# Performance work log

Hardware: AMD Instinct MI355X
Metric: run time of the kernel (lower is better)

## Reference

```python
import jax, jax.numpy as jnp
import numpy as np

H, W = 32, 32
DIM = 768
NUM_BLOCKS = 4
BLOCK = DIM // NUM_BLOCKS
SCALE = 0.02


def setup_inputs() -> dict:
    key = jax.random.key(0)
    k0, k1, k2, k3, k4 = jax.random.split(key, 5)
    B, N, C = 64, H * W, DIM
    x = jax.random.normal(k0, (B, N, C), dtype=jnp.float32)
    w1 = SCALE * jax.random.normal(k1, (2, NUM_BLOCKS, BLOCK, BLOCK), dtype=jnp.float32)
    b1 = SCALE * jax.random.normal(k2, (2, NUM_BLOCKS, BLOCK), dtype=jnp.float32)
    w2 = SCALE * jax.random.normal(k3, (2, NUM_BLOCKS, BLOCK, BLOCK), dtype=jnp.float32)
    b2 = SCALE * jax.random.normal(k4, (2, NUM_BLOCKS, BLOCK), dtype=jnp.float32)
    return {"x": x, "w1": w1, "b1": b1, "w2": w2, "b2": b2}


def _mul(inp, weights):
    # inp: [B, H, Wf, blocks, d], weights: [blocks, d, k]
    return jnp.einsum('...bd,bdk->...bk', inp, weights)


def reference(x, w1, b1, w2, b2):
    B, N, C = x.shape
    xg = x.reshape(B, H, W, C)
    xf = jnp.fft.rfft2(xg, axes=(1, 2), norm='ortho')  # [B, H, W//2+1, C] complex64
    xf = xf.reshape(B, xf.shape[1], xf.shape[2], NUM_BLOCKS, BLOCK)
    xr, xi = xf.real, xf.imag
    # layer 1: complex block-diagonal linear + ReLU
    r1 = jax.nn.relu(_mul(xr, w1[0]) - _mul(xi, w1[1]) + b1[0])
    i1 = jax.nn.relu(_mul(xr, w1[1]) + _mul(xi, w1[0]) + b1[1])
    # layer 2 (faithful to original: imag uses the already-updated real part)
    r2 = _mul(r1, w2[0]) - _mul(i1, w2[1]) + b2[0]
    i2 = _mul(r2, w2[1]) + _mul(i1, w2[0]) + b2[1]
    xc = (r2 + 1j * i2).reshape(B, r2.shape[1], r2.shape[2], C)
    out = jnp.fft.irfft2(xc, s=(H, W), axes=(1, 2), norm='ortho')
    return out.reshape(B, N, C) + jnp.zeros_like(x)  # bias is zeros (self.bias is None)
```

## Files before the change

### kernel.cpp

```cpp
#include <hip/hip_runtime.h>
#include <cstddef>
#include <cstdint>


typedef __attribute__((ext_vector_type(8))) short bf16x8;
typedef __attribute__((ext_vector_type(4))) float f32x4;

namespace {

constexpr int BATCH = 64;
constexpr int WF    = 17;
constexpr int CC    = 768;
constexpr int BLK   = 192;

constexpr size_t W_ELEMS  = 16u * 36864u;
constexpr size_t TW_ELEMS = 8u * 1024u;
constexpr size_t PW_ELEMS = W_ELEMS + TW_ELEMS;

constexpr int PLANE_U = 48 * 512;

constexpr float C32[32] = {
   1.0000000000f,  0.9807852804f,  0.9238795325f,  0.8314696123f,
   0.7071067812f,  0.5555702330f,  0.3826834324f,  0.1950903220f,
   0.0000000000f, -0.1950903220f, -0.3826834324f, -0.5555702330f,
  -0.7071067812f, -0.8314696123f, -0.9238795325f, -0.9807852804f,
  -1.0000000000f, -0.9807852804f, -0.9238795325f, -0.8314696123f,
  -0.7071067812f, -0.5555702330f, -0.3826834324f, -0.1950903220f,
   0.0000000000f,  0.1950903220f,  0.3826834324f,  0.5555702330f,
   0.7071067812f,  0.8314696123f,  0.9238795325f,  0.9807852804f
};
constexpr float S32[32] = {
   0.0000000000f,  0.1950903220f,  0.3826834324f,  0.5555702330f,
   0.7071067812f,  0.8314696123f,  0.9238795325f,  0.9807852804f,
   1.0000000000f,  0.9807852804f,  0.9238795325f,  0.8314696123f,
   0.7071067812f,  0.5555702330f,  0.3826834324f,  0.1950903220f,
   0.0000000000f, -0.1950903220f, -0.3826834324f, -0.5555702330f,
  -0.7071067812f, -0.8314696123f, -0.9238795325f, -0.9807852804f,
  -1.0000000000f, -0.9807852804f, -0.9238795325f, -0.8314696123f,
  -0.7071067812f, -0.5555702330f, -0.3826834324f, -0.1950903220f
};

}

__device__ __forceinline__ ushort f2bf(float f) {
    union { float f; unsigned u; } v; v.f = f;
    const unsigned r = (v.u + 0x7FFFu + ((v.u >> 16) & 1u)) >> 16;
    return (ushort)r;
}
__device__ __forceinline__ uint pk(float lo, float hi) {
    return (uint)f2bf(lo) | ((uint)f2bf(hi) << 16);
}
__device__ __forceinline__ bf16x8 neg8(bf16x8 a) {
    union { bf16x8 v; uint4 u; } t; t.v = a;
    t.u.x ^= 0x80008000u; t.u.y ^= 0x80008000u;
    t.u.z ^= 0x80008000u; t.u.w ^= 0x80008000u;
    return t.v;
}

__global__ __launch_bounds__(256) void k_pack(const float* __restrict__ w1,
                                              const float* __restrict__ w2,
                                              ushort* __restrict__ pw) {
    const unsigned idx = blockIdx.x * 256u + threadIdx.x;
    if (idx < W_ELEMS) {
        const unsigned mi = idx / 36864u;
        const unsigned r  = idx % 36864u;
        const unsigned kk = r / 6144u;
        const unsigned r2 = r % 6144u;
        const unsigned nf = r2 / 512u;
        const unsigned r3 = r2 % 512u;
        const unsigned lane = r3 / 8u;
        const unsigned i  = r3 % 8u;
        const unsigned d   = kk * 32u + (lane >> 4) * 8u + i;
        const unsigned col = nf * 16u + (lane & 15u);
        const unsigned mat = mi >> 2, blk = mi & 3u;
        const float* src;
        if      (mat == 0u) src = w1 + (size_t)(0 * 4 + blk) * BLK * BLK;
        else if (mat == 1u) src = w1 + (size_t)(1 * 4 + blk) * BLK * BLK;
        else if (mat == 2u) src = w2 + (size_t)(0 * 4 + blk) * BLK * BLK;
        else                src = w2 + (size_t)(1 * 4 + blk) * BLK * BLK;
        pw[idx] = f2bf(src[(size_t)d * BLK + col]);
    } else if (idx < PW_ELEMS) {
        const unsigned t = idx - (unsigned)W_ELEMS;
        const unsigned mat = t >> 10;
        const unsigned rr  = t & 1023u;
        const unsigned mf  = rr >> 9;
        const unsigned q   = rr & 511u;
        const unsigned lane = q >> 3, i = q & 7u;
        const unsigned row = mf * 16u + (lane & 15u);
        const unsigned col = (lane >> 4) * 8u + i;
        const unsigned ang = (row * col) & 31u;
        float v;
        if      (mat == 0u) v = C32[ang] * 0.03125f;
        else if (mat == 1u) v = S32[ang] * 0.03125f;
        else if (mat == 2u) v = -S32[ang] * 0.03125f;
        else if (mat == 3u) v = C32[ang];
        else if (mat == 4u) v = S32[ang];
        else if (mat == 5u) v = -S32[ang];
        else if (mat == 6u) {
            if      (col == 0u)  v = 0.03125f;
            else if (col < 16u)  v = 2.f * C32[ang] * 0.03125f;
            else if (col == 16u) v = C32[(16u * row) & 31u] * 0.03125f;
            else                 v = 0.f;
        } else {
            v = (col >= 1u && col <= 15u) ? (-2.f * S32[ang] * 0.03125f) : 0.f;
        }
        pw[idx] = f2bf(v);
    }
}

__global__ __launch_bounds__(256) void k_rfft_w(const float* __restrict__ x,
                                                ushort* __restrict__ spec,
                                                const ushort* __restrict__ pw) {
    __shared__ uint xb[16 * 384];

    const int bid = blockIdx.x;
    const int cq = bid & 3;
    const int hp = (bid >> 2) & 15;
    const int b  = bid >> 6;
    const int tid = threadIdx.x;
    const int wv = tid >> 6, l = tid & 63, lc = l & 15, lg = l >> 4;

#pragma unroll
    for (int it = 0; it < 6; ++it) {
        const int flat = it * 256 + tid;
        const int h  = flat / 768;
        const int rm = flat % 768;
        const int wp = rm / 48;
        const int c4 = rm % 48;
        const float* p = x + ((size_t)(b * 1024 + (hp * 2 + h) * 32 + wp * 2) * CC)
                           + cq * 192 + c4 * 4;
        const float4 a  = *(const float4*)p;
        const float4 bb = *(const float4*)(p + CC);
        uint4 u;
        u.x = pk(a.x, bb.x); u.y = pk(a.y, bb.y);
        u.z = pk(a.z, bb.z); u.w = pk(a.w, bb.w);
        const int col = (h * 192 + c4 * 4) ^ (((wp >> 2) & 3) << 3);
        *(uint4*)&xb[wp * 384 + col] = u;
    }
    __syncthreads();

    const ushort* TW = pw + W_ELEMS;
    bf16x8 ac[2], as[2];
#pragma unroll
    for (int m = 0; m < 2; ++m) {
        ac[m] = *(const bf16x8*)(TW + ((size_t)(3 * 2 + m) * 64 + l) * 8);
        as[m] = *(const bf16x8*)(TW + ((size_t)(5 * 2 + m) * 64 + l) * 8);
    }

    f32x4 aR[2][6] = {}, aI[2][6] = {};
#pragma unroll
    for (int j = 0; j < 6; ++j) {
        const int nf = (j < 3) ? (wv * 3 + j) : (12 + wv * 3 + (j - 3));
        union { bf16x8 v; uint d[4]; } u;
#pragma unroll
        for (int t = 0; t < 4; ++t) {
            const int wp = lg * 4 + t;
            u.d[t] = xb[wp * 384 + ((nf * 16 + lc) ^ (lg << 3))];
        }
#pragma unroll
        for (int m = 0; m < 2; ++m) {
            aR[m][j] = __builtin_amdgcn_mfma_f32_16x16x32_bf16(ac[m], u.v, aR[m][j], 0, 0, 0);
            aI[m][j] = __builtin_amdgcn_mfma_f32_16x16x32_bf16(as[m], u.v, aI[m][j], 0, 0, 0);
        }
    }

    uint* spec32 = (uint*)spec;
    const int swz = (hp & 7) << 1;
#pragma unroll
    for (int m = 0; m < 2; ++m)
#pragma unroll
        for (int j = 0; j < 3; ++j)
#pragma unroll
            for (int r = 0; r < 4; ++r) {
                if (m == 1 && (lg != 0 || r != 0)) continue;
                const int kw = m * 16 + lg * 4 + r;
                const int csub = cq * 12 + wv * 3 + j;
                const size_t pos = ((size_t)(b * WF + kw) * 2) * 12288
                                 + csub * 256 + hp * 16 + (lc ^ swz);
                spec32[pos]         = pk(aR[m][j][r], aR[m][j + 3][r]);
                spec32[pos + 12288] = pk(aI[m][j][r], aI[m][j + 3][r]);
            }
}

__global__ __launch_bounds__(256, 4) void k_fft_mix(
        ushort* __restrict__ spec,
        const ushort* __restrict__ pw,
        const float* __restrict__ b1, const float* __restrict__ b2) {

    __shared__ ushort lds[3][6336];

    const int bid = blockIdx.x;
    const int blk = bid / (BATCH * WF);
    const int rem = bid % (BATCH * WF);
    const int b   = rem / WF;
    const int kw  = rem % WF;
    const int tid = threadIdx.x;
    const int wv = tid >> 6, l = tid & 63, lc = l & 15, lg = l >> 4;

    const size_t gR = ((size_t)(b * WF + kw) * 2) * PLANE_U + blk * 6144;
    const size_t gI = gR + PLANE_U;

#pragma unroll
    for (int j = 0; j < 3; ++j) {
        const int q = tid + 256 * j;
        const int dst = (q >> 6) * 528 + (q & 63) * 8;
        *(uint4*)&lds[0][dst] = *(const uint4*)(spec + gR + q * 8);
        *(uint4*)&lds[1][dst] = *(const uint4*)(spec + gI + q * 8);
    }
    __syncthreads();

    const ushort* TW = pw + W_ELEMS;
    const int col0 = wv * 48;

    {
        bf16x8 xr[3], xi[3];
#pragma unroll
        for (int n = 0; n < 3; ++n) {
            const int csub = wv * 3 + n;
            union { bf16x8 v; uint d[4]; } ur, ui;
#pragma unroll
            for (int t = 0; t < 4; ++t) {
                const int hp = lg * 4 + t;
                const int pos = csub * 528 + hp * 32 + ((lc ^ ((hp & 7) << 1)) << 1);
                ur.d[t] = *(const uint*)&lds[0][pos];
                ui.d[t] = *(const uint*)&lds[1][pos];
            }
            xr[n] = ur.v; xi[n] = ui.v;
        }
        bf16x8 cf[2], sf[2], sfn[2];
#pragma unroll
        for (int m = 0; m < 2; ++m) {
            cf[m]  = *(const bf16x8*)(TW + ((size_t)(0 * 2 + m) * 64 + l) * 8);
            sf[m]  = *(const bf16x8*)(TW + ((size_t)(1 * 2 + m) * 64 + l) * 8);
            sfn[m] = *(const bf16x8*)(TW + ((size_t)(2 * 2 + m) * 64 + l) * 8);
        }
        f32x4 yr[2][3] = {}, yi[2][3] = {};
#pragma unroll
        for (int m = 0; m < 2; ++m)
#pragma unroll
            for (int n = 0; n < 3; ++n) {
                yr[m][n] = __builtin_amdgcn_mfma_f32_16x16x32_bf16(cf[m],  xr[n], yr[m][n], 0, 0, 0);
                yr[m][n] = __builtin_amdgcn_mfma_f32_16x16x32_bf16(sf[m],  xi[n], yr[m][n], 0, 0, 0);
                yi[m][n] = __builtin_amdgcn_mfma_f32_16x16x32_bf16(cf[m],  xi[n], yi[m][n], 0, 0, 0);
                yi[m][n] = __builtin_amdgcn_mfma_f32_16x16x32_bf16(sfn[m], xr[n], yi[m][n], 0, 0, 0);
            }
#pragma unroll
        for (int m = 0; m < 2; ++m)
#pragma unroll
            for (int n = 0; n < 3; ++n)
#pragma unroll
                for (int rp = 0; rp < 2; ++rp) {
                    const uint ur = pk(yr[m][n][2 * rp], yr[m][n][2 * rp + 1]);
                    const uint ui = pk(yi[m][n][2 * rp], yi[m][n][2 * rp + 1]);
                    const int p0 = (wv * 3 + n) * 528 + (m * 16 + lg * 4 + 2 * rp) * 16 + lc;
                    lds[0][p0] = (ushort)ur; lds[0][p0 + 16] = (ushort)(ur >> 16);
                    lds[1][p0] = (ushort)ui; lds[1][p0 + 16] = (ushort)(ui >> 16);
                }
    }
    __syncthreads();

    const ushort* pW1r = pw + (size_t)(0 * 4 + blk) * 36864;
    const ushort* pW1i = pw + (size_t)(1 * 4 + blk) * 36864;
    const ushort* pW2r = pw + (size_t)(2 * 4 + blk) * 36864;
    const ushort* pW2i = pw + (size_t)(3 * 4 + blk) * 36864;

    {
        f32x4 aR[2][3], aI[2][3];
#pragma unroll
        for (int n = 0; n < 3; ++n) {
            const float br = b1[(size_t)(0 * 4 + blk) * BLK + col0 + n * 16 + lc];
            const float bi = b1[(size_t)(1 * 4 + blk) * BLK + col0 + n * 16 + lc];
#pragma unroll
            for (int m = 0; m < 2; ++m) {
                aR[m][n] = (f32x4){br, br, br, br};
                aI[m][n] = (f32x4){bi, bi, bi, bi};
            }
        }
#pragma unroll
        for (int kk = 0; kk < 6; ++kk) {
            const int csubA = 2 * kk + (lg >> 1);
            const int apos  = csubA * 528 + lc * 16 + (lg & 1) * 8;
            bf16x8 ar[2], ai[2], ain[2];
#pragma unroll
            for (int m = 0; m < 2; ++m) {
                ar[m]  = *(const bf16x8*)&lds[0][apos + m * 256];
                ai[m]  = *(const bf16x8*)&lds[1][apos + m * 256];
                ain[m] = neg8(ai[m]);
            }
            bf16x8 wr[3], wi[3];
#pragma unroll
            for (int n = 0; n < 3; ++n) {
                const size_t off = ((size_t)(kk * 12 + wv * 3 + n) * 64 + l) * 8;
                wr[n] = *(const bf16x8*)(pW1r + off);
                wi[n] = *(const bf16x8*)(pW1i + off);
            }
#pragma unroll
            for (int m = 0; m < 2; ++m)
#pragma unroll
                for (int n = 0; n < 3; ++n) {
                    aR[m][n] = __builtin_amdgcn_mfma_f32_16x16x32_bf16(ar[m],  wr[n], aR[m][n], 0, 0, 0);
                    aR[m][n] = __builtin_amdgcn_mfma_f32_16x16x32_bf16(ain[m], wi[n], aR[m][n], 0, 0, 0);
                    aI[m][n] = __builtin_amdgcn_mfma_f32_16x16x32_bf16(ar[m],  wi[n], aI[m][n], 0, 0, 0);
                    aI[m][n] = __builtin_amdgcn_mfma_f32_16x16x32_bf16(ai[m],  wr[n], aI[m][n], 0, 0, 0);
                }
        }
        __syncthreads();
#pragma unroll
        for (int m = 0; m < 2; ++m)
#pragma unroll
            for (int n = 0; n < 3; ++n)
#pragma unroll
                for (int rp = 0; rp < 2; ++rp) {
                    const uint ur = pk(fmaxf(aR[m][n][2 * rp], 0.f), fmaxf(aR[m][n][2 * rp + 1], 0.f));
                    const uint ui = pk(fmaxf(aI[m][n][2 * rp], 0.f), fmaxf(aI[m][n][2 * rp + 1], 0.f));
                    const int p0 = (wv * 3 + n) * 528 + (m * 16 + lg * 4 + 2 * rp) * 16 + lc;
                    lds[0][p0] = (ushort)ur; lds[0][p0 + 16] = (ushort)(ur >> 16);
                    lds[1][p0] = (ushort)ui; lds[1][p0 + 16] = (ushort)(ui >> 16);
                }
    }
    __syncthreads();

    {
        f32x4 cR[2][3];
#pragma unroll
        for (int n = 0; n < 3; ++n) {
            const float br = b2[(size_t)(0 * 4 + blk) * BLK + col0 + n * 16 + lc];
#pragma unroll
            for (int m = 0; m < 2; ++m) cR[m][n] = (f32x4){br, br, br, br};
        }
#pragma unroll
        for (int kk = 0; kk < 6; ++kk) {
            const int csubA = 2 * kk + (lg >> 1);
            const int apos  = csubA * 528 + lc * 16 + (lg & 1) * 8;
            bf16x8 ar[2], ain[2];
#pragma unroll
            for (int m = 0; m < 2; ++m) {
                ar[m]  = *(const bf16x8*)&lds[0][apos + m * 256];
                ain[m] = neg8(*(const bf16x8*)&lds[1][apos + m * 256]);
            }
            bf16x8 wr[3], wi[3];
#pragma unroll
            for (int n = 0; n < 3; ++n) {
                const size_t off = ((size_t)(kk * 12 + wv * 3 + n) * 64 + l) * 8;
                wr[n] = *(const bf16x8*)(pW2r + off);
                wi[n] = *(const bf16x8*)(pW2i + off);
            }
#pragma unroll
            for (int m = 0; m < 2; ++m)
#pragma unroll
                for (int n = 0; n < 3; ++n) {
                    cR[m][n] = __builtin_amdgcn_mfma_f32_16x16x32_bf16(ar[m],  wr[n], cR[m][n], 0, 0, 0);
                    cR[m][n] = __builtin_amdgcn_mfma_f32_16x16x32_bf16(ain[m], wi[n], cR[m][n], 0, 0, 0);
                }
        }
        __syncthreads();
#pragma unroll
        for (int m = 0; m < 2; ++m)
#pragma unroll
            for (int n = 0; n < 3; ++n) {
                const int csub = wv * 3 + n;
#pragma unroll
                for (int rp = 0; rp < 2; ++rp) {
                    const uint p = pk(cR[m][n][2 * rp], cR[m][n][2 * rp + 1]);
                    const int kh0 = m * 16 + lg * 4 + 2 * rp;
                    lds[0][csub * 528 + kh0 * 16 + lc]       = (ushort)p;
                    lds[0][csub * 528 + (kh0 + 1) * 16 + lc] = (ushort)(p >> 16);
                    const int hp = kh0 >> 1;
                    const int post = csub * 528 + hp * 32 + ((lc ^ ((hp & 7) << 1)) << 1);
                    *(uint*)&lds[2][post] = p;
                }
            }
    }
    __syncthreads();

    {
        f32x4 cI[2][3];
#pragma unroll
        for (int n = 0; n < 3; ++n) {
            const float bi = b2[(size_t)(1 * 4 + blk) * BLK + col0 + n * 16 + lc];
#pragma unroll
            for (int m = 0; m < 2; ++m) cI[m][n] = (f32x4){bi, bi, bi, bi};
        }
#pragma unroll
        for (int kk = 0; kk < 6; ++kk) {
            const int csubA = 2 * kk + (lg >> 1);
            const int apos  = csubA * 528 + lc * 16 + (lg & 1) * 8;
            bf16x8 a2[2], i1[2];
#pragma unroll
            for (int m = 0; m < 2; ++m) {
                a2[m] = *(const bf16x8*)&lds[0][apos + m * 256];
                i1[m] = *(const bf16x8*)&lds[1][apos + m * 256];
            }
            bf16x8 wi[3], wr[3];
#pragma unroll
            for (int n = 0; n < 3; ++n) {
                const size_t off = ((size_t)(kk * 12 + wv * 3 + n) * 64 + l) * 8;
                wi[n] = *(const bf16x8*)(pW2i + off);
                wr[n] = *(const bf16x8*)(pW2r + off);
            }
#pragma unroll
            for (int m = 0; m < 2; ++m)
#pragma unroll
                for (int n = 0; n < 3; ++n) {
                    cI[m][n] = __builtin_amdgcn_mfma_f32_16x16x32_bf16(a2[m], wi[n], cI[m][n], 0, 0, 0);
                    cI[m][n] = __builtin_amdgcn_mfma_f32_16x16x32_bf16(i1[m], wr[n], cI[m][n], 0, 0, 0);
                }
        }
        __syncthreads();
#pragma unroll
        for (int m = 0; m < 2; ++m)
#pragma unroll
            for (int n = 0; n < 3; ++n) {
                const int csub = wv * 3 + n;
#pragma unroll
                for (int rp = 0; rp < 2; ++rp) {
                    const int hp = (m * 16 + lg * 4 + 2 * rp) >> 1;
                    const int post = csub * 528 + hp * 32 + ((lc ^ ((hp & 7) << 1)) << 1);
                    *(uint*)&lds[1][post] = pk(cI[m][n][2 * rp], cI[m][n][2 * rp + 1]);
                }
            }
    }

    {
        bf16x8 ci[2], si[2], sn[2];
#pragma unroll
        for (int m = 0; m < 2; ++m) {
            ci[m] = *(const bf16x8*)(TW + ((size_t)(3 * 2 + m) * 64 + l) * 8);
            si[m] = *(const bf16x8*)(TW + ((size_t)(4 * 2 + m) * 64 + l) * 8);
            sn[m] = *(const bf16x8*)(TW + ((size_t)(5 * 2 + m) * 64 + l) * 8);
        }
        bf16x8 r2b[3], i2b[3];
#pragma unroll
        for (int n = 0; n < 3; ++n) {
            const int csub = wv * 3 + n;
            union { bf16x8 v; uint d[4]; } ur, ui;
#pragma unroll
            for (int t = 0; t < 4; ++t) {
                const int hp = lg * 4 + t;
                const int pos = csub * 528 + hp * 32 + ((lc ^ ((hp & 7) << 1)) << 1);
                ur.d[t] = *(const uint*)&lds[2][pos];
                ui.d[t] = *(const uint*)&lds[1][pos];
            }
            r2b[n] = ur.v; i2b[n] = ui.v;
        }
        f32x4 zr[2][3] = {}, zi[2][3] = {};
#pragma unroll
        for (int m = 0; m < 2; ++m)
#pragma unroll
            for (int n = 0; n < 3; ++n) {
                zr[m][n] = __builtin_amdgcn_mfma_f32_16x16x32_bf16(ci[m], r2b[n], zr[m][n], 0, 0, 0);
                zr[m][n] = __builtin_amdgcn_mfma_f32_16x16x32_bf16(sn[m], i2b[n], zr[m][n], 0, 0, 0);
                zi[m][n] = __builtin_amdgcn_mfma_f32_16x16x32_bf16(ci[m], i2b[n], zi[m][n], 0, 0, 0);
                zi[m][n] = __builtin_amdgcn_mfma_f32_16x16x32_bf16(si[m], r2b[n], zi[m][n], 0, 0, 0);
            }
#pragma unroll
        for (int m = 0; m < 2; ++m)
#pragma unroll
            for (int n = 0; n < 3; ++n) {
                const size_t cbase = gR + (size_t)(wv * 3 + n) * 512;
#pragma unroll
                for (int rp = 0; rp < 2; ++rp) {
                    const int hp = (m * 16 + lg * 4 + 2 * rp) >> 1;
                    const size_t pos = cbase + hp * 32 + ((lc ^ ((hp & 7) << 1)) << 1);
                    *(uint*)(spec + pos)           = pk(zr[m][n][2 * rp], zr[m][n][2 * rp + 1]);
                    *(uint*)(spec + pos + PLANE_U) = pk(zi[m][n][2 * rp], zi[m][n][2 * rp + 1]);
                }
            }
    }
}

__global__ __launch_bounds__(256) void k_irfft_w(const ushort* __restrict__ spec,
                                                 float* __restrict__ out,
                                                 const ushort* __restrict__ pw) {
    __shared__ uint rawR[17 * 198];
    __shared__ uint rawI[17 * 198];

    const int bid = blockIdx.x;
    const int cq = bid & 3;
    const int hp = (bid >> 2) & 15;
    const int b  = bid >> 6;
    const int tid = threadIdx.x;
    const int wv = tid >> 6, l = tid & 63, lc = l & 15, lg = l >> 4;

    const uint* spec32 = (const uint*)spec;

#pragma unroll
    for (int it = 0; it < 13; ++it) {
        const int slot = it * 256 + tid;
        if (slot < 3264) {
            const int part = slot & 7;
            const int c2   = slot >> 3;
            const int plane = c2 / 204;
            const int q  = c2 % 204;
            const int kw = q / 12, csub = q % 12;
            const size_t gpos = ((size_t)(b * WF + kw) * 2 + plane) * 12288
                              + (cq * 12 + csub) * 256 + hp * 16 + part * 2;
            const uint2 v = *(const uint2*)(spec32 + gpos);
            uint* dst = plane ? rawI : rawR;
            *(uint2*)&dst[kw * 198 + csub * 16 + part * 2] = v;
        }
    }
    __syncthreads();

    const ushort* TW = pw + W_ELEMS;
    bf16x8 twA[2], twB[2];
#pragma unroll
    for (int m = 0; m < 2; ++m) {
        twA[m] = *(const bf16x8*)(TW + ((size_t)(6 * 2 + m) * 64 + l) * 8);
        twB[m] = *(const bf16x8*)(TW + ((size_t)(7 * 2 + m) * 64 + l) * 8);
    }

    int rowoff[8];
#pragma unroll
    for (int i = 0; i < 8; ++i) {
        int kwv = lg * 8 + i;
        if (kwv > 16) kwv = 16;
        rowoff[i] = kwv * 396;
    }

    const ushort* rr = (const ushort*)rawR;
    const ushort* ri = (const ushort*)rawI;
    const int swz = (hp & 7) << 1;

    f32x4 acc[2][6] = {};
#pragma unroll
    for (int j = 0; j < 6; ++j) {
        const int coll = (wv * 6 + j) * 16 + lc;
        const int h  = coll & 1;
        const int cL = coll >> 1;
        const int bu = ((cL >> 4) * 16 + ((cL & 15) ^ swz)) * 2 + h;
        union { bf16x8 v; ushort s[8]; } fr, fi;
#pragma unroll
        for (int i = 0; i < 8; ++i) {
            fr.s[i] = rr[rowoff[i] + bu];
            fi.s[i] = ri[rowoff[i] + bu];
        }
#pragma unroll
        for (int m = 0; m < 2; ++m) {
            acc[m][j] = __builtin_amdgcn_mfma_f32_16x16x32_bf16(twA[m], fr.v, acc[m][j], 0, 0, 0);
            acc[m][j] = __builtin_amdgcn_mfma_f32_16x16x32_bf16(twB[m], fi.v, acc[m][j], 0, 0, 0);
        }
    }

#pragma unroll
    for (int m = 0; m < 2; ++m)
#pragma unroll
        for (int j = 0; j < 6; ++j) {
            const int coll = (wv * 6 + j) * 16 + lc;
            const int h  = coll & 1;
            const int c  = cq * 192 + (coll >> 1);
#pragma unroll
            for (int r = 0; r < 4; ++r) {
                const int w = m * 16 + lg * 4 + r;
                out[((size_t)(b * 1024 + (hp * 2 + h) * 32 + w)) * CC + c] = acc[m][j][r];
            }
        }
}

extern "C" void kernel_launch(void* const* d_in, const int* in_sizes, int n_in,
                              void* d_out, int out_size, void* d_ws, size_t ws_size,
                              hipStream_t stream) {
    const float* x  = (const float*)d_in[0];
    const float* w1 = (const float*)d_in[1];
    const float* b1 = (const float*)d_in[2];
    const float* w2 = (const float*)d_in[3];
    const float* b2 = (const float*)d_in[4];
    float* out = (float*)d_out;

    ushort* pw   = (ushort*)d_ws;
    ushort* spec = pw + PW_ELEMS;

    k_pack<<<dim3((unsigned)(PW_ELEMS / 256)), dim3(256), 0, stream>>>(w1, w2, pw);
    k_rfft_w<<<dim3(BATCH * 16 * 4), dim3(256), 0, stream>>>(x, spec, pw);
    k_fft_mix<<<dim3(4 * BATCH * WF), dim3(256), 0, stream>>>(spec, pw, b1, b2);
    k_irfft_w<<<dim3(BATCH * 16 * 4), dim3(256), 0, stream>>>(spec, out, pw);
}
```

Measured before the change: 285.5 us.

## Add fourth LDS buffer to drop barriers; derive negated twiddles in registers

Grows the fused spectral-mix kernel's shared memory from three to four bf16 planes so layer-1 outputs go to separate buffers. This lets two __syncthreads after the layer-2 GEMM loops be removed, since writes no longer overwrite data other waves may still be reading. It also drops the occupancy hint from launch_bounds and computes negated sine twiddles with neg8 instead of loading them. The larger LDS footprint and missing occupancy hint may cut the number of resident blocks per CU.

```diff
diff --git a/kernel.cpp b/kernel.cpp
--- a/kernel.cpp
+++ b/kernel.cpp
@@ -182,12 +182,12 @@
             }
 }
 
-__global__ __launch_bounds__(256, 4) void k_fft_mix(
+__global__ __launch_bounds__(256) void k_fft_mix(
         ushort* __restrict__ spec,
         const ushort* __restrict__ pw,
         const float* __restrict__ b1, const float* __restrict__ b2) {
 
-    __shared__ ushort lds[3][6336];
+    __shared__ ushort lds[4][6336];
 
     const int bid = blockIdx.x;
     const int blk = bid / (BATCH * WF);
@@ -232,7 +232,7 @@
         for (int m = 0; m < 2; ++m) {
             cf[m]  = *(const bf16x8*)(TW + ((size_t)(0 * 2 + m) * 64 + l) * 8);
             sf[m]  = *(const bf16x8*)(TW + ((size_t)(1 * 2 + m) * 64 + l) * 8);
-            sfn[m] = *(const bf16x8*)(TW + ((size_t)(2 * 2 + m) * 64 + l) * 8);
+            sfn[m] = neg8(sf[m]);
         }
         f32x4 yr[2][3] = {}, yi[2][3] = {};
 #pragma unroll
@@ -249,12 +249,10 @@
 #pragma unroll
             for (int n = 0; n < 3; ++n)
 #pragma unroll
-                for (int rp = 0; rp < 2; ++rp) {
-                    const uint ur = pk(yr[m][n][2 * rp], yr[m][n][2 * rp + 1]);
-                    const uint ui = pk(yi[m][n][2 * rp], yi[m][n][2 * rp + 1]);
-                    const int p0 = (wv * 3 + n) * 528 + (m * 16 + lg * 4 + 2 * rp) * 16 + lc;
-                    lds[0][p0] = (ushort)ur; lds[0][p0 + 16] = (ushort)(ur >> 16);
-                    lds[1][p0] = (ushort)ui; lds[1][p0 + 16] = (ushort)(ui >> 16);
+                for (int r = 0; r < 4; ++r) {
+                    const int pos = (wv * 3 + n) * 528 + (m * 16 + lg * 4 + r) * 16 + lc;
+                    lds[0][pos] = f2bf(yr[m][n][r]);
+                    lds[1][pos] = f2bf(yi[m][n][r]);
                 }
     }
     __syncthreads();
@@ -310,12 +308,12 @@
 #pragma unroll
             for (int n = 0; n < 3; ++n)
 #pragma unroll
-                for (int rp = 0; rp < 2; ++rp) {
-                    const uint ur = pk(fmaxf(aR[m][n][2 * rp], 0.f), fmaxf(aR[m][n][2 * rp + 1], 0.f));
-                    const uint ui = pk(fmaxf(aI[m][n][2 * rp], 0.f), fmaxf(aI[m][n][2 * rp + 1], 0.f));
-                    const int p0 = (wv * 3 + n) * 528 + (m * 16 + lg * 4 + 2 * rp) * 16 + lc;
-                    lds[0][p0] = (ushort)ur; lds[0][p0 + 16] = (ushort)(ur >> 16);
-                    lds[1][p0] = (ushort)ui; lds[1][p0 + 16] = (ushort)(ui >> 16);
+                for (int r = 0; r < 4; ++r) {
+                    float rv = aR[m][n][r]; rv = rv > 0.f ? rv : 0.f;
+                    float iv = aI[m][n][r]; iv = iv > 0.f ? iv : 0.f;
+                    const int pos = (wv * 3 + n) * 528 + (m * 16 + lg * 4 + r) * 16 + lc;
+                    lds[2][pos] = f2bf(rv);
+                    lds[3][pos] = f2bf(iv);
                 }
     }
     __syncthreads();
@@ -335,8 +333,8 @@
             bf16x8 ar[2], ain[2];
 #pragma unroll
             for (int m = 0; m < 2; ++m) {
-                ar[m]  = *(const bf16x8*)&lds[0][apos + m * 256];
-                ain[m] = neg8(*(const bf16x8*)&lds[1][apos + m * 256]);
+                ar[m]  = *(const bf16x8*)&lds[2][apos + m * 256];
+                ain[m] = neg8(*(const bf16x8*)&lds[3][apos + m * 256]);
             }
             bf16x8 wr[3], wi[3];
 #pragma unroll
@@ -353,7 +351,6 @@
                     cR[m][n] = __builtin_amdgcn_mfma_f32_16x16x32_bf16(ain[m], wi[n], cR[m][n], 0, 0, 0);
                 }
         }
-        __syncthreads();
 #pragma unroll
         for (int m = 0; m < 2; ++m)
 #pragma unroll
@@ -361,20 +358,21 @@
                 const int csub = wv * 3 + n;
 #pragma unroll
                 for (int rp = 0; rp < 2; ++rp) {
-                    const uint p = pk(cR[m][n][2 * rp], cR[m][n][2 * rp + 1]);
+                    const ushort lo = f2bf(cR[m][n][2 * rp]);
+                    const ushort hi = f2bf(cR[m][n][2 * rp + 1]);
                     const int kh0 = m * 16 + lg * 4 + 2 * rp;
-                    lds[0][csub * 528 + kh0 * 16 + lc]       = (ushort)p;
-                    lds[0][csub * 528 + (kh0 + 1) * 16 + lc] = (ushort)(p >> 16);
+                    lds[0][csub * 528 + kh0 * 16 + lc]       = lo;
+                    lds[0][csub * 528 + (kh0 + 1) * 16 + lc] = hi;
                     const int hp = kh0 >> 1;
                     const int post = csub * 528 + hp * 32 + ((lc ^ ((hp & 7) << 1)) << 1);
-                    *(uint*)&lds[2][post] = p;
+                    *(uint*)&lds[1][post] = (uint)lo | ((uint)hi << 16);
                 }
             }
     }
     __syncthreads();
 
+    f32x4 cI[2][3];
     {
-        f32x4 cI[2][3];
 #pragma unroll
         for (int n = 0; n < 3; ++n) {
             const float bi = b2[(size_t)(1 * 4 + blk) * BLK + col0 + n * 16 + lc];
@@ -389,14 +387,14 @@
 #pragma unroll
             for (int m = 0; m < 2; ++m) {
                 a2[m] = *(const bf16x8*)&lds[0][apos + m * 256];
-                i1[m] = *(const bf16x8*)&lds[1][apos + m * 256];
-            }
-            bf16x8 wi[3], wr[3];
+                i1[m] = *(const bf16x8*)&lds[3][apos + m * 256];
+            }
+            bf16x8 wr[3], wi[3];
 #pragma unroll
             for (int n = 0; n < 3; ++n) {
                 const size_t off = ((size_t)(kk * 12 + wv * 3 + n) * 64 + l) * 8;
+                wr[n] = *(const bf16x8*)(pW2r + off);
                 wi[n] = *(const bf16x8*)(pW2i + off);
-                wr[n] = *(const bf16x8*)(pW2r + off);
             }
 #pragma unroll
             for (int m = 0; m < 2; ++m)
@@ -406,7 +404,6 @@
                     cI[m][n] = __builtin_amdgcn_mfma_f32_16x16x32_bf16(i1[m], wr[n], cI[m][n], 0, 0, 0);
                 }
         }
-        __syncthreads();
 #pragma unroll
         for (int m = 0; m < 2; ++m)
 #pragma unroll
@@ -416,18 +413,19 @@
                 for (int rp = 0; rp < 2; ++rp) {
                     const int hp = (m * 16 + lg * 4 + 2 * rp) >> 1;
                     const int post = csub * 528 + hp * 32 + ((lc ^ ((hp & 7) << 1)) << 1);
-                    *(uint*)&lds[1][post] = pk(cI[m][n][2 * rp], cI[m][n][2 * rp + 1]);
+                    *(uint*)&lds[2][post] =
+                        (uint)f2bf(cI[m][n][2 * rp]) | ((uint)f2bf(cI[m][n][2 * rp + 1]) << 16);
                 }
             }
     }
 
     {
-        bf16x8 ci[2], si[2], sn[2];
+        bf16x8 ci[2], si[2], sin_[2];
 #pragma unroll
         for (int m = 0; m < 2; ++m) {
-            ci[m] = *(const bf16x8*)(TW + ((size_t)(3 * 2 + m) * 64 + l) * 8);
-            si[m] = *(const bf16x8*)(TW + ((size_t)(4 * 2 + m) * 64 + l) * 8);
-            sn[m] = *(const bf16x8*)(TW + ((size_t)(5 * 2 + m) * 64 + l) * 8);
+            ci[m]   = *(const bf16x8*)(TW + ((size_t)(3 * 2 + m) * 64 + l) * 8);
+            si[m]   = *(const bf16x8*)(TW + ((size_t)(4 * 2 + m) * 64 + l) * 8);
+            sin_[m] = neg8(si[m]);
         }
         bf16x8 r2b[3], i2b[3];
 #pragma unroll
@@ -438,8 +436,8 @@
             for (int t = 0; t < 4; ++t) {
                 const int hp = lg * 4 + t;
                 const int pos = csub * 528 + hp * 32 + ((lc ^ ((hp & 7) << 1)) << 1);
-                ur.d[t] = *(const uint*)&lds[2][pos];
-                ui.d[t] = *(const uint*)&lds[1][pos];
+                ur.d[t] = *(const uint*)&lds[1][pos];
+                ui.d[t] = *(const uint*)&lds[2][pos];
             }
             r2b[n] = ur.v; i2b[n] = ui.v;
         }
@@ -448,10 +446,10 @@
         for (int m = 0; m < 2; ++m)
 #pragma unroll
             for (int n = 0; n < 3; ++n) {
-                zr[m][n] = __builtin_amdgcn_mfma_f32_16x16x32_bf16(ci[m], r2b[n], zr[m][n], 0, 0, 0);
-                zr[m][n] = __builtin_amdgcn_mfma_f32_16x16x32_bf16(sn[m], i2b[n], zr[m][n], 0, 0, 0);
-                zi[m][n] = __builtin_amdgcn_mfma_f32_16x16x32_bf16(ci[m], i2b[n], zi[m][n], 0, 0, 0);
-                zi[m][n] = __builtin_amdgcn_mfma_f32_16x16x32_bf16(si[m], r2b[n], zi[m][n], 0, 0, 0);
+                zr[m][n] = __builtin_amdgcn_mfma_f32_16x16x32_bf16(ci[m],   r2b[n], zr[m][n], 0, 0, 0);
+                zr[m][n] = __builtin_amdgcn_mfma_f32_16x16x32_bf16(sin_[m], i2b[n], zr[m][n], 0, 0, 0);
+                zi[m][n] = __builtin_amdgcn_mfma_f32_16x16x32_bf16(ci[m],   i2b[n], zi[m][n], 0, 0, 0);
+                zi[m][n] = __builtin_amdgcn_mfma_f32_16x16x32_bf16(si[m],   r2b[n], zi[m][n], 0, 0, 0);
             }
 #pragma unroll
         for (int m = 0; m < 2; ++m)
@@ -462,8 +460,10 @@
                 for (int rp = 0; rp < 2; ++rp) {
                     const int hp = (m * 16 + lg * 4 + 2 * rp) >> 1;
                     const size_t pos = cbase + hp * 32 + ((lc ^ ((hp & 7) << 1)) << 1);
-                    *(uint*)(spec + pos)           = pk(zr[m][n][2 * rp], zr[m][n][2 * rp + 1]);
-                    *(uint*)(spec + pos + PLANE_U) = pk(zi[m][n][2 * rp], zi[m][n][2 * rp + 1]);
+                    *(uint*)(spec + pos) =
+                        (uint)f2bf(zr[m][n][2 * rp]) | ((uint)f2bf(zr[m][n][2 * rp + 1]) << 16);
+                    *(uint*)(spec + pos + PLANE_U) =
+                        (uint)f2bf(zi[m][n][2 * rp]) | ((uint)f2bf(zi[m][n][2 * rp + 1]) << 16);
                 }
             }
     }
```

Result: faster. 259.2 us (-9.2%).
